# Kernel optimization log

Measured on AMD Instinct MI355X. Metric: run time of the kernel, lower is better.

## Reference

```python
import jax, jax.numpy as jnp
import numpy as np

B, D, K, S = 8192, 1024, 8192, 64  # batch, feature_dim, num_blocks, block_size
EPS = 1e-5


def layer_norm(x, g, b):
    mu = jnp.mean(x, axis=-1, keepdims=True)
    var = jnp.var(x, axis=-1, keepdims=True)
    return (x - mu) * jax.lax.rsqrt(var + EPS) * g + b


def setup_inputs() -> dict:
    key = jax.random.key(0)
    ks = jax.random.split(key, 12)
    s = 0.02
    return {
        "features": jax.random.normal(ks[0], (B, D), dtype=jnp.float32),
        "codebook": jax.random.normal(ks[1], (K, S), dtype=jnp.float32) * 0.1,
        # projection: Linear(D, 2S) -> ReLU -> LayerNorm(2S) -> Linear(2S, S)
        "proj_w1": jax.random.normal(ks[2], (D, 2 * S), dtype=jnp.float32) * s,
        "proj_b1": jnp.zeros((2 * S,), dtype=jnp.float32),
        "ln1_g": jnp.ones((2 * S,), dtype=jnp.float32),
        "ln1_b": jnp.zeros((2 * S,), dtype=jnp.float32),
        "proj_w2": jax.random.normal(ks[3], (2 * S, S), dtype=jnp.float32) * s,
        "proj_b2": jnp.zeros((S,), dtype=jnp.float32),
        # reconstruction: Linear(S, 2D) -> ReLU -> LayerNorm(2D) -> Linear(2D, D)
        "rec_w1": jax.random.normal(ks[4], (S, 2 * D), dtype=jnp.float32) * s,
        "rec_b1": jnp.zeros((2 * D,), dtype=jnp.float32),
        "ln2_g": jnp.ones((2 * D,), dtype=jnp.float32),
        "ln2_b": jnp.zeros((2 * D,), dtype=jnp.float32),
        "rec_w2": jax.random.normal(ks[5], (2 * D, D), dtype=jnp.float32) * s,
        "rec_b2": jnp.zeros((D,), dtype=jnp.float32),
    }


def reference(features, codebook, proj_w1, proj_b1, ln1_g, ln1_b, proj_w2, proj_b2,
              rec_w1, rec_b1, ln2_g, ln2_b, rec_w2, rec_b2):
    # --- encode ---
    h = jax.nn.relu(features @ proj_w1 + proj_b1)
    h = layer_norm(h, ln1_g, ln1_b)
    z = h @ proj_w2 + proj_b2  # [B, S] (dropout inactive in eval)
    # squared Euclidean distances; argmin identical to cdist(p=2) argmin
    d2 = (jnp.sum(z * z, axis=1, keepdims=True)
          - 2.0 * (z @ codebook.T)
          + jnp.sum(codebook * codebook, axis=1))  # [B, K]
    indices = jnp.argmin(d2, axis=1)  # [B]
    # usage scatter-add (buffer update in the torch module)
    block_usage = jnp.zeros((K,), dtype=jnp.float32).at[indices].add(1.0)
    # --- decode ---
    sel = codebook[indices]  # [B, S] embedding gather
    r = jax.nn.relu(sel @ rec_w1 + rec_b1)
    r = layer_norm(r, ln2_g, ln2_b)
    reconstructed = r @ rec_w2 + rec_b2  # [B, D]
    return reconstructed, indices, block_usage
```

## Files before the change

kernel.cpp:

```cpp
#include <hip/hip_runtime.h>
#include <hip/hip_bf16.h>
#include <stdint.h>

#define LN_EPS 1e-5f

typedef float f32x4 __attribute__((ext_vector_type(4)));
typedef short short8 __attribute__((ext_vector_type(8)));

__device__ __forceinline__ float bf2f(unsigned int u) {
  union { unsigned int i; float f; } x; x.i = u << 16; return x.f;
}
__device__ __forceinline__ unsigned short f2bf(float f) {
  unsigned int x = __float_as_uint(f);
  x += 0x7fffu + ((x >> 16) & 1u);
  return (unsigned short)(x >> 16);
}

__device__ __forceinline__ void gload16(const void* g, void* l) {
  __builtin_amdgcn_global_load_lds((const __attribute__((address_space(1))) unsigned int*)g,
                                   (__attribute__((address_space(3))) unsigned int*)l, 16, 0, 0);
}

__device__ __forceinline__ void stage_tile(const unsigned short* g, int ldg,
                                           unsigned short* lds, int wave, int lane) {
#pragma unroll
  for (int i = 0; i < 4; i++) {
    const int chunk = i * 4 + wave;
    const unsigned short* ga = g + (size_t)(chunk * 8 + (lane >> 3)) * ldg + (lane & 7) * 8;
    gload16(ga, lds + chunk * 512);
  }
}

__global__ __launch_bounds__(256) void k0_c2_zero(const float* __restrict__ CB,
                                                  float* __restrict__ C2,
                                                  float* __restrict__ usage) {
  const int g = blockIdx.x * 256 + threadIdx.x;
  const int code = g >> 4, l16 = g & 15;
  const float4 v = *(const float4*)&CB[(size_t)code * 64 + (l16 << 2)];
  float s = v.x * v.x + v.y * v.y + v.z * v.z + v.w * v.w;
#pragma unroll
  for (int m = 8; m >= 1; m >>= 1) s += __shfl_xor(s, m, 16);
  if (l16 == 0) C2[code] = s;
  if (g < 8192) usage[g] = 0.f;
}

__global__ __launch_bounds__(256) void k1_encode(const float* __restrict__ X,
                                                 const float* __restrict__ W1,
                                                 const float* __restrict__ B1,
                                                 const float* __restrict__ G1,
                                                 const float* __restrict__ Bn1,
                                                 const float* __restrict__ W2,
                                                 const float* __restrict__ B2,
                                                 float* __restrict__ Z) {
  __shared__ float At[64][20];
  __shared__ float Wc[64][128];
  __shared__ float Ht[128][20];
  const int t = threadIdx.x;
  const int row0 = blockIdx.x << 4;
  const int rg = t >> 6;
  const int r0 = rg << 2;
  const int cg = t & 63;
  const int c0 = cg << 1;
  const int lr = t >> 4, lkc = (t & 15) << 2;
  float acc[4][2] = {{0,0},{0,0},{0,0},{0,0}};

  for (int k0 = 0; k0 < 1024; k0 += 64) {
    __syncthreads();
    {
      const float4 av = *(const float4*)&X[(size_t)(row0 + lr) * 1024 + k0 + lkc];
      At[lkc + 0][lr] = av.x; At[lkc + 1][lr] = av.y;
      At[lkc + 2][lr] = av.z; At[lkc + 3][lr] = av.w;
    }
    {
      const float4* wsrc = (const float4*)&W1[(size_t)k0 * 128];
      float4* wdst = (float4*)&Wc[0][0];
#pragma unroll
      for (int i = 0; i < 8; i++) wdst[t + (i << 8)] = wsrc[t + (i << 8)];
    }
    __syncthreads();
#pragma unroll
    for (int kk = 0; kk < 64; kk++) {
      const float4 a = *(const float4*)&At[kk][r0];
      const float2 w = *(const float2*)&Wc[kk][c0];
      acc[0][0] = fmaf(a.x, w.x, acc[0][0]); acc[0][1] = fmaf(a.x, w.y, acc[0][1]);
      acc[1][0] = fmaf(a.y, w.x, acc[1][0]); acc[1][1] = fmaf(a.y, w.y, acc[1][1]);
      acc[2][0] = fmaf(a.z, w.x, acc[2][0]); acc[2][1] = fmaf(a.z, w.y, acc[2][1]);
      acc[3][0] = fmaf(a.w, w.x, acc[3][0]); acc[3][1] = fmaf(a.w, w.y, acc[3][1]);
    }
  }
  const float b1a = B1[c0], b1b = B1[c0 + 1];
  float h[4][2], s1[4], s2[4];
#pragma unroll
  for (int i = 0; i < 4; i++) {
    h[i][0] = fmaxf(acc[i][0] + b1a, 0.f);
    h[i][1] = fmaxf(acc[i][1] + b1b, 0.f);
    s1[i] = h[i][0] + h[i][1];
    s2[i] = h[i][0] * h[i][0] + h[i][1] * h[i][1];
  }
#pragma unroll
  for (int m = 32; m >= 1; m >>= 1) {
#pragma unroll
    for (int i = 0; i < 4; i++) { s1[i] += __shfl_xor(s1[i], m); s2[i] += __shfl_xor(s2[i], m); }
  }
  const float ga = G1[c0], gb = G1[c0 + 1], ba = Bn1[c0], bb = Bn1[c0 + 1];
#pragma unroll
  for (int i = 0; i < 4; i++) {
    const float mean = s1[i] * (1.f / 128.f);
    const float var  = s2[i] * (1.f / 128.f) - mean * mean;
    const float rs = rsqrtf(var + LN_EPS);
    Ht[c0 + 0][r0 + i] = (h[i][0] - mean) * rs * ga + ba;
    Ht[c0 + 1][r0 + i] = (h[i][1] - mean) * rs * gb + bb;
  }
  __syncthreads();
  float za[4] = {0, 0, 0, 0};
  for (int k = 0; k < 128; k++) {
    const float4 hv = *(const float4*)&Ht[k][r0];
    const float wv = W2[(k << 6) + cg];
    za[0] = fmaf(hv.x, wv, za[0]); za[1] = fmaf(hv.y, wv, za[1]);
    za[2] = fmaf(hv.z, wv, za[2]); za[3] = fmaf(hv.w, wv, za[3]);
  }
  const float b2v = B2[cg];
#pragma unroll
  for (int i = 0; i < 4; i++)
    Z[(size_t)(row0 + r0 + i) * 64 + cg] = za[i] + b2v;
}

__global__ __launch_bounds__(256) void k2_dist(const float* __restrict__ Z,
                                               const float* __restrict__ CB,
                                               const float* __restrict__ C2,
                                               float* __restrict__ Pval,
                                               int* __restrict__ Pidx) {
  __shared__ float Zt[64][36];
  __shared__ float Ct[2][64][132];
  const int t = threadIdx.x;
  const int lane = t & 63, wave = t >> 6;
  const int rowblk = blockIdx.x >> 1, half = blockIdx.x & 1;
  const int row0 = rowblk << 5;
  const int code0 = half << 12;
  const int rg = t >> 5;
  const int r0 = rg << 2;
  const int c0 = (lane & 31) << 2;

#pragma unroll
  for (int i = 0; i < 2; i++) {
    const int f = t + (i << 8);
    const int r = f >> 4, kc = (f & 15) << 2;
    const float4 v = *(const float4*)&Z[(size_t)(row0 + r) * 64 + kc];
    Zt[kc + 0][r] = v.x; Zt[kc + 1][r] = v.y;
    Zt[kc + 2][r] = v.z; Zt[kc + 3][r] = v.w;
  }

  const int wq = (wave << 4) + (lane >> 2);
  const int kb = (lane & 3) << 2;
  float4 st[8];
#define K2_PF(cr, r) \
  st[(cr) * 4 + (r)] = *(const float4*)&CB[(size_t)(code0 + chunk * 128 + (cr) * 64 + wq) * 64 + kb + 16 * (r)];
#define K2_WR(cr, r) { \
    const float4 v = st[(cr) * 4 + (r)]; \
    const int k2r = kb + 16 * (r); const int col = (cr) * 64 + wq; \
    Ct[buf][k2r + 0][col] = v.x; Ct[buf][k2r + 1][col] = v.y; \
    Ct[buf][k2r + 2][col] = v.z; Ct[buf][k2r + 3][col] = v.w; }

  {
    const int chunk = 0;
    K2_PF(0, 0) K2_PF(0, 1) K2_PF(0, 2) K2_PF(0, 3)
    K2_PF(1, 0) K2_PF(1, 1) K2_PF(1, 2) K2_PF(1, 3)
  }
  __syncthreads();

  float minv[4] = {3.4e38f, 3.4e38f, 3.4e38f, 3.4e38f};
  int   mini[4] = {0, 0, 0, 0};

  for (int c = 0; c < 32; c++) {
    const int buf = c & 1;
    K2_WR(0, 0) K2_WR(0, 1) K2_WR(0, 2) K2_WR(0, 3)
    K2_WR(1, 0) K2_WR(1, 1) K2_WR(1, 2) K2_WR(1, 3)
    __syncthreads();
    if (c + 1 < 32) {
      const int chunk = c + 1;
      K2_PF(0, 0) K2_PF(0, 1) K2_PF(0, 2) K2_PF(0, 3)
      K2_PF(1, 0) K2_PF(1, 1) K2_PF(1, 2) K2_PF(1, 3)
    }
    float acc[4][4];
#pragma unroll
    for (int i = 0; i < 4; i++)
#pragma unroll
      for (int j = 0; j < 4; j++) acc[i][j] = 0.f;
#pragma unroll 4
    for (int k = 0; k < 64; k++) {
      const float4 zv = *(const float4*)&Zt[k][r0];
      const float4 cv = *(const float4*)&Ct[buf][k][c0];
      acc[0][0] = fmaf(zv.x, cv.x, acc[0][0]); acc[0][1] = fmaf(zv.x, cv.y, acc[0][1]);
      acc[0][2] = fmaf(zv.x, cv.z, acc[0][2]); acc[0][3] = fmaf(zv.x, cv.w, acc[0][3]);
      acc[1][0] = fmaf(zv.y, cv.x, acc[1][0]); acc[1][1] = fmaf(zv.y, cv.y, acc[1][1]);
      acc[1][2] = fmaf(zv.y, cv.z, acc[1][2]); acc[1][3] = fmaf(zv.y, cv.w, acc[1][3]);
      acc[2][0] = fmaf(zv.z, cv.x, acc[2][0]); acc[2][1] = fmaf(zv.z, cv.y, acc[2][1]);
      acc[2][2] = fmaf(zv.z, cv.z, acc[2][2]); acc[2][3] = fmaf(zv.z, cv.w, acc[2][3]);
      acc[3][0] = fmaf(zv.w, cv.x, acc[3][0]); acc[3][1] = fmaf(zv.w, cv.y, acc[3][1]);
      acc[3][2] = fmaf(zv.w, cv.z, acc[3][2]); acc[3][3] = fmaf(zv.w, cv.w, acc[3][3]);
    }
    const int codeb = code0 + (c << 7) + c0;
    const float4 c2v = *(const float4*)&C2[codeb];
    const float c2a[4] = {c2v.x, c2v.y, c2v.z, c2v.w};
#pragma unroll
    for (int i = 0; i < 4; i++)
#pragma unroll
      for (int j = 0; j < 4; j++) {
        const float s = fmaf(-2.f, acc[i][j], c2a[j]);
        if (s < minv[i]) { minv[i] = s; mini[i] = codeb + j; }
      }
  }
#undef K2_PF
#undef K2_WR
#pragma unroll
  for (int m = 16; m >= 1; m >>= 1) {
#pragma unroll
    for (int i = 0; i < 4; i++) {
      const float ov = __shfl_xor(minv[i], m);
      const int   oi = __shfl_xor(mini[i], m);
      if (ov < minv[i] || (ov == minv[i] && oi < mini[i])) { minv[i] = ov; mini[i] = oi; }
    }
  }
  if ((lane & 31) == 0) {
#pragma unroll
    for (int i = 0; i < 4; i++) {
      const int r = row0 + r0 + i;
      Pval[r * 2 + half] = minv[i];
      Pidx[r * 2 + half] = mini[i];
    }
  }
}

__global__ __launch_bounds__(256) void k2_merge(const float* __restrict__ Pval,
                                                const int* __restrict__ Pidx,
                                                int* __restrict__ IDX,
                                                float* __restrict__ outIdx,
                                                float* __restrict__ usage) {
  const int r = blockIdx.x * 256 + threadIdx.x;
  const float v0 = Pval[r * 2], v1 = Pval[r * 2 + 1];
  const int i0 = Pidx[r * 2], i1 = Pidx[r * 2 + 1];
  const int best = (v1 < v0) ? i1 : i0;
  IDX[r] = best;
  outIdx[r] = (float)best;
  atomicAdd(&usage[best], 1.0f);
}

__global__ __launch_bounds__(256) void k_tcast(const float* __restrict__ src,
                                               unsigned short* __restrict__ dst,
                                               int R, int C) {
  __shared__ float T[32][33];
  const int tilesC = C >> 5;
  const int bx = blockIdx.x;
  const int tr = bx / tilesC, tc = bx - tr * tilesC;
  const int t = threadIdx.x;
  {
    const int r = t >> 3, c4 = (t & 7) << 2;
    const float4 v = *(const float4*)&src[(size_t)(tr * 32 + r) * C + tc * 32 + c4];
    T[r][c4] = v.x; T[r][c4 + 1] = v.y; T[r][c4 + 2] = v.z; T[r][c4 + 3] = v.w;
  }
  __syncthreads();
  const int c = t >> 3, r4 = (t & 7) << 2;
  ushort4 o;
  o.x = f2bf(T[r4 + 0][c]); o.y = f2bf(T[r4 + 1][c]);
  o.z = f2bf(T[r4 + 2][c]); o.w = f2bf(T[r4 + 3][c]);
  *(ushort4*)&dst[(size_t)(tc * 32 + c) * R + tr * 32 + r4] = o;
}

__global__ __launch_bounds__(256) void k3_gather(const float* __restrict__ CB,
                                                 const int* __restrict__ IDX,
                                                 unsigned short* __restrict__ SEL) {
  const int g = blockIdx.x * 256 + threadIdx.x;
  const int row = g >> 4, c4 = (g & 15) << 2;
  const int code = IDX[row];
  const float4 v = *(const float4*)&CB[(size_t)code * 64 + c4];
  ushort4 o;
  o.x = f2bf(v.x); o.y = f2bf(v.y); o.z = f2bf(v.z); o.w = f2bf(v.w);
  *(ushort4*)&SEL[(size_t)row * 64 + c4] = o;
}

__global__ __launch_bounds__(256) void k4_rec1(const unsigned short* __restrict__ A,
                                               const unsigned short* __restrict__ Bt,
                                               const float* __restrict__ bias,
                                               unsigned short* __restrict__ H) {
  __shared__ __align__(16) unsigned short As[128 * 64];
  __shared__ __align__(16) unsigned short Bs[128 * 64];
  const int t = threadIdx.x;
  const int wave = t >> 6, lane = t & 63;
  const int bx = blockIdx.x;
  const int tm = bx >> 4, tn = bx & 15;
  const int m0 = tm << 7, n0 = tn << 7;
  const int wm = wave >> 1, wn = wave & 1;
  const int ln15 = lane & 15, lk = (lane >> 4) << 3;
  stage_tile(A + (size_t)m0 * 64, 64, As, wave, lane);
  stage_tile(Bt + (size_t)n0 * 64, 64, Bs, wave, lane);
  asm volatile("s_waitcnt vmcnt(0)" ::: "memory");
  __syncthreads();
  f32x4 acc[4][4];
#pragma unroll
  for (int i = 0; i < 4; i++)
#pragma unroll
    for (int j = 0; j < 4; j++) acc[i][j] = (f32x4){0.f, 0.f, 0.f, 0.f};
#pragma unroll
  for (int ks = 0; ks < 2; ks++) {
    short8 a[4], b[4];
#pragma unroll
    for (int i = 0; i < 4; i++)
      a[i] = *(const short8*)&As[(wm * 64 + i * 16 + ln15) * 64 + ks * 32 + lk];
#pragma unroll
    for (int j = 0; j < 4; j++)
      b[j] = *(const short8*)&Bs[(wn * 64 + j * 16 + ln15) * 64 + ks * 32 + lk];
#pragma unroll
    for (int i = 0; i < 4; i++)
#pragma unroll
      for (int j = 0; j < 4; j++)
        acc[i][j] = __builtin_amdgcn_mfma_f32_16x16x32_bf16(a[i], b[j], acc[i][j], 0, 0, 0);
  }
  const int l4 = (lane >> 4) << 2;
#pragma unroll
  for (int j = 0; j < 4; j++) {
    const int col = n0 + wn * 64 + j * 16 + ln15;
    const float bv = bias[col];
#pragma unroll
    for (int i = 0; i < 4; i++) {
      const int row = m0 + wm * 64 + i * 16 + l4;
#pragma unroll
      for (int r = 0; r < 4; r++)
        H[(size_t)(row + r) * 2048 + col] = f2bf(fmaxf(acc[i][j][r] + bv, 0.f));
    }
  }
}

__global__ __launch_bounds__(256) void k5_ln(unsigned short* __restrict__ H,
                                             const float* __restrict__ G,
                                             const float* __restrict__ B) {
  const int row = blockIdx.x, t = threadIdx.x;
  unsigned short* p = H + (size_t)row * 2048 + t * 8;
  const uint4 raw = *(const uint4*)p;
  float v[8];
  v[0] = bf2f(raw.x & 0xffffu); v[1] = bf2f(raw.x >> 16);
  v[2] = bf2f(raw.y & 0xffffu); v[3] = bf2f(raw.y >> 16);
  v[4] = bf2f(raw.z & 0xffffu); v[5] = bf2f(raw.z >> 16);
  v[6] = bf2f(raw.w & 0xffffu); v[7] = bf2f(raw.w >> 16);
  float s1 = 0.f, s2 = 0.f;
#pragma unroll
  for (int i = 0; i < 8; i++) { s1 += v[i]; s2 = fmaf(v[i], v[i], s2); }
#pragma unroll
  for (int m = 32; m >= 1; m >>= 1) { s1 += __shfl_xor(s1, m); s2 += __shfl_xor(s2, m); }
  __shared__ float red[8];
  const int lane = t & 63, wv = t >> 6;
  if (lane == 0) { red[wv] = s1; red[4 + wv] = s2; }
  __syncthreads();
  s1 = red[0] + red[1] + red[2] + red[3];
  s2 = red[4] + red[5] + red[6] + red[7];
  const float mean = s1 * (1.f / 2048.f);
  const float var  = s2 * (1.f / 2048.f) - mean * mean;
  const float rs = rsqrtf(var + LN_EPS);
  const int c = t * 8;
  unsigned int w0, w1, w2, w3;
  {
    const float o0 = (v[0] - mean) * rs * G[c + 0] + B[c + 0];
    const float o1 = (v[1] - mean) * rs * G[c + 1] + B[c + 1];
    w0 = (unsigned int)f2bf(o0) | ((unsigned int)f2bf(o1) << 16);
  }
  {
    const float o0 = (v[2] - mean) * rs * G[c + 2] + B[c + 2];
    const float o1 = (v[3] - mean) * rs * G[c + 3] + B[c + 3];
    w1 = (unsigned int)f2bf(o0) | ((unsigned int)f2bf(o1) << 16);
  }
  {
    const float o0 = (v[4] - mean) * rs * G[c + 4] + B[c + 4];
    const float o1 = (v[5] - mean) * rs * G[c + 5] + B[c + 5];
    w2 = (unsigned int)f2bf(o0) | ((unsigned int)f2bf(o1) << 16);
  }
  {
    const float o0 = (v[6] - mean) * rs * G[c + 6] + B[c + 6];
    const float o1 = (v[7] - mean) * rs * G[c + 7] + B[c + 7];
    w3 = (unsigned int)f2bf(o0) | ((unsigned int)f2bf(o1) << 16);
  }
  uint4 outw; outw.x = w0; outw.y = w1; outw.z = w2; outw.w = w3;
  *(uint4*)p = outw;
}

__global__ __launch_bounds__(256) void k6_rec2(const unsigned short* __restrict__ A,
                                               const unsigned short* __restrict__ Bt,
                                               const float* __restrict__ bias,
                                               float* __restrict__ C) {
  __shared__ __align__(16) unsigned short As[128 * 64];
  __shared__ __align__(16) unsigned short Bs[128 * 64];
  const int t = threadIdx.x;
  const int wave = t >> 6, lane = t & 63;
  const int bx = blockIdx.x;
  const int tm = bx >> 3, tn = bx & 7;
  const int m0 = tm << 7, n0 = tn << 7;
  const int wm = wave >> 1, wn = wave & 1;
  const int ln15 = lane & 15, lk = (lane >> 4) << 3;
  f32x4 acc[4][4];
#pragma unroll
  for (int i = 0; i < 4; i++)
#pragma unroll
    for (int j = 0; j < 4; j++) acc[i][j] = (f32x4){0.f, 0.f, 0.f, 0.f};

  for (int k0 = 0; k0 < 2048; k0 += 64) {
    __syncthreads();
    stage_tile(A + (size_t)m0 * 2048 + k0, 2048, As, wave, lane);
    stage_tile(Bt + (size_t)n0 * 2048 + k0, 2048, Bs, wave, lane);
    asm volatile("s_waitcnt vmcnt(0)" ::: "memory");
    __syncthreads();
#pragma unroll
    for (int ks = 0; ks < 2; ks++) {
      short8 a[4], b[4];
#pragma unroll
      for (int i = 0; i < 4; i++)
        a[i] = *(const short8*)&As[(wm * 64 + i * 16 + ln15) * 64 + ks * 32 + lk];
#pragma unroll
      for (int j = 0; j < 4; j++)
        b[j] = *(const short8*)&Bs[(wn * 64 + j * 16 + ln15) * 64 + ks * 32 + lk];
#pragma unroll
      for (int i = 0; i < 4; i++)
#pragma unroll
        for (int j = 0; j < 4; j++)
          acc[i][j] = __builtin_amdgcn_mfma_f32_16x16x32_bf16(a[i], b[j], acc[i][j], 0, 0, 0);
    }
  }
  const int l4 = (lane >> 4) << 2;
#pragma unroll
  for (int j = 0; j < 4; j++) {
    const int col = n0 + wn * 64 + j * 16 + ln15;
    const float bv = bias[col];
#pragma unroll
    for (int i = 0; i < 4; i++) {
      const int row = m0 + wm * 64 + i * 16 + l4;
#pragma unroll
      for (int r = 0; r < 4; r++)
        C[(size_t)(row + r) * 1024 + col] = acc[i][j][r] + bv;
    }
  }
}

extern "C" void kernel_launch(void* const* d_in, const int* in_sizes, int n_in,
                              void* d_out, int out_size, void* d_ws, size_t ws_size,
                              hipStream_t stream) {
  (void)in_sizes; (void)n_in; (void)out_size; (void)ws_size;
  const float* features = (const float*)d_in[0];
  const float* codebook = (const float*)d_in[1];
  const float* proj_w1  = (const float*)d_in[2];
  const float* proj_b1  = (const float*)d_in[3];
  const float* ln1_g    = (const float*)d_in[4];
  const float* ln1_b    = (const float*)d_in[5];
  const float* proj_w2  = (const float*)d_in[6];
  const float* proj_b2  = (const float*)d_in[7];
  const float* rec_w1   = (const float*)d_in[8];
  const float* rec_b1   = (const float*)d_in[9];
  const float* ln2_g    = (const float*)d_in[10];
  const float* ln2_b    = (const float*)d_in[11];
  const float* rec_w2   = (const float*)d_in[12];
  const float* rec_b2   = (const float*)d_in[13];

  float* out_recon = (float*)d_out;
  float* out_idx   = out_recon + (size_t)8192 * 1024;
  float* out_usage = out_idx + 8192;

  char* ws = (char*)d_ws;
  float*          c2  = (float*)(ws);
  int*            idx = (int*)(ws + 32768);
  float*          z   = (float*)(ws + 65536);
  unsigned short* sel = (unsigned short*)(ws + 2162688);
  unsigned short* w1t = (unsigned short*)(ws + 3211264);
  unsigned short* w2t = (unsigned short*)(ws + 3473408);
  unsigned short* h1  = (unsigned short*)(ws + 7667712);
  float* pval = (float*)(ws + 2162688);
  int*   pidx = (int*)(ws + 2162688 + 65536);

  k0_c2_zero<<<512, 256, 0, stream>>>(codebook, c2, out_usage);
  k1_encode <<<512, 256, 0, stream>>>(features, proj_w1, proj_b1, ln1_g, ln1_b,
                                      proj_w2, proj_b2, z);
  k2_dist   <<<512, 256, 0, stream>>>(z, codebook, c2, pval, pidx);
  k2_merge  <<<32, 256, 0, stream>>>(pval, pidx, idx, out_idx, out_usage);
  k_tcast   <<<128, 256, 0, stream>>>(rec_w1, w1t, 64, 2048);
  k_tcast   <<<2048, 256, 0, stream>>>(rec_w2, w2t, 2048, 1024);
  k3_gather <<<512, 256, 0, stream>>>(codebook, idx, sel);
  k4_rec1   <<<1024, 256, 0, stream>>>(sel, w1t, rec_b1, h1);
  k5_ln     <<<8192, 256, 0, stream>>>(h1, ln2_g, ln2_b);
  k6_rec2   <<<512, 256, 0, stream>>>(h1, w2t, rec_b2, out_recon);
}
```

Before: 396.5 us.

## Split distance search into four code quarters and double-buffer rec2 GEMM tiles

The distance kernel now splits the codebook into four quarters per row block instead of two, which doubles the grid to 1024 blocks. Its LDS tile becomes single-buffered with an extra barrier, cutting shared memory per block so more blocks can be resident. The merge kernel reduces four partial minima using vector loads. The rec2 MFMA GEMM gains double-buffered LDS staging so the next K tile loads while the current one computes, at the cost of twice the LDS footprint.

```diff
diff --git a/kernel.cpp b/kernel.cpp
--- a/kernel.cpp
+++ b/kernel.cpp
@@ -130,15 +130,14 @@
                                                const float* __restrict__ C2,
                                                float* __restrict__ Pval,
                                                int* __restrict__ Pidx) {
-  __shared__ float Zt[64][36];
-  __shared__ float Ct[2][64][132];
+  __shared__ float Zt[64][34];
+  __shared__ float Ct[64][130];
   const int t = threadIdx.x;
   const int lane = t & 63, wave = t >> 6;
-  const int rowblk = blockIdx.x >> 1, half = blockIdx.x & 1;
+  const int rowblk = blockIdx.x >> 2, quarter = blockIdx.x & 3;
   const int row0 = rowblk << 5;
-  const int code0 = half << 12;
-  const int rg = t >> 5;
-  const int r0 = rg << 2;
+  const int code0 = quarter << 11;
+  const int r0 = (t >> 5) << 2;
   const int c0 = (lane & 31) << 2;
 
 #pragma unroll
@@ -158,8 +157,8 @@
 #define K2_WR(cr, r) { \
     const float4 v = st[(cr) * 4 + (r)]; \
     const int k2r = kb + 16 * (r); const int col = (cr) * 64 + wq; \
-    Ct[buf][k2r + 0][col] = v.x; Ct[buf][k2r + 1][col] = v.y; \
-    Ct[buf][k2r + 2][col] = v.z; Ct[buf][k2r + 3][col] = v.w; }
+    Ct[k2r + 0][col] = v.x; Ct[k2r + 1][col] = v.y; \
+    Ct[k2r + 2][col] = v.z; Ct[k2r + 3][col] = v.w; }
 
   {
     const int chunk = 0;
@@ -171,12 +170,11 @@
   float minv[4] = {3.4e38f, 3.4e38f, 3.4e38f, 3.4e38f};
   int   mini[4] = {0, 0, 0, 0};
 
-  for (int c = 0; c < 32; c++) {
-    const int buf = c & 1;
+  for (int c = 0; c < 16; c++) {
     K2_WR(0, 0) K2_WR(0, 1) K2_WR(0, 2) K2_WR(0, 3)
     K2_WR(1, 0) K2_WR(1, 1) K2_WR(1, 2) K2_WR(1, 3)
     __syncthreads();
-    if (c + 1 < 32) {
+    if (c + 1 < 16) {
       const int chunk = c + 1;
       K2_PF(0, 0) K2_PF(0, 1) K2_PF(0, 2) K2_PF(0, 3)
       K2_PF(1, 0) K2_PF(1, 1) K2_PF(1, 2) K2_PF(1, 3)
@@ -189,7 +187,7 @@
 #pragma unroll 4
     for (int k = 0; k < 64; k++) {
       const float4 zv = *(const float4*)&Zt[k][r0];
-      const float4 cv = *(const float4*)&Ct[buf][k][c0];
+      const float4 cv = *(const float4*)&Ct[k][c0];
       acc[0][0] = fmaf(zv.x, cv.x, acc[0][0]); acc[0][1] = fmaf(zv.x, cv.y, acc[0][1]);
       acc[0][2] = fmaf(zv.x, cv.z, acc[0][2]); acc[0][3] = fmaf(zv.x, cv.w, acc[0][3]);
       acc[1][0] = fmaf(zv.y, cv.x, acc[1][0]); acc[1][1] = fmaf(zv.y, cv.y, acc[1][1]);
@@ -209,6 +207,7 @@
         const float s = fmaf(-2.f, acc[i][j], c2a[j]);
         if (s < minv[i]) { minv[i] = s; mini[i] = codeb + j; }
       }
+    __syncthreads();
   }
 #undef K2_PF
 #undef K2_WR
@@ -225,8 +224,8 @@
 #pragma unroll
     for (int i = 0; i < 4; i++) {
       const int r = row0 + r0 + i;
-      Pval[r * 2 + half] = minv[i];
-      Pidx[r * 2 + half] = mini[i];
+      Pval[r * 4 + quarter] = minv[i];
+      Pidx[r * 4 + quarter] = mini[i];
     }
   }
 }
@@ -237,12 +236,15 @@
                                                 float* __restrict__ outIdx,
                                                 float* __restrict__ usage) {
   const int r = blockIdx.x * 256 + threadIdx.x;
-  const float v0 = Pval[r * 2], v1 = Pval[r * 2 + 1];
-  const int i0 = Pidx[r * 2], i1 = Pidx[r * 2 + 1];
-  const int best = (v1 < v0) ? i1 : i0;
-  IDX[r] = best;
-  outIdx[r] = (float)best;
-  atomicAdd(&usage[best], 1.0f);
+  const float4 v = *(const float4*)&Pval[r * 4];
+  const int4   i = *(const int4*)&Pidx[r * 4];
+  float bv = v.x; int bi = i.x;
+  if (v.y < bv) { bv = v.y; bi = i.y; }
+  if (v.z < bv) { bv = v.z; bi = i.z; }
+  if (v.w < bv) { bv = v.w; bi = i.w; }
+  IDX[r] = bi;
+  outIdx[r] = (float)bi;
+  atomicAdd(&usage[bi], 1.0f);
 }
 
 __global__ __launch_bounds__(256) void k_tcast(const float* __restrict__ src,
@@ -385,8 +387,8 @@
                                                const unsigned short* __restrict__ Bt,
                                                const float* __restrict__ bias,
                                                float* __restrict__ C) {
-  __shared__ __align__(16) unsigned short As[128 * 64];
-  __shared__ __align__(16) unsigned short Bs[128 * 64];
+  __shared__ __align__(16) unsigned short As[2][128 * 64];
+  __shared__ __align__(16) unsigned short Bs[2][128 * 64];
   const int t = threadIdx.x;
   const int wave = t >> 6, lane = t & 63;
   const int bx = blockIdx.x;
@@ -400,27 +402,36 @@
 #pragma unroll
     for (int j = 0; j < 4; j++) acc[i][j] = (f32x4){0.f, 0.f, 0.f, 0.f};
 
-  for (int k0 = 0; k0 < 2048; k0 += 64) {
-    __syncthreads();
-    stage_tile(A + (size_t)m0 * 2048 + k0, 2048, As, wave, lane);
-    stage_tile(Bt + (size_t)n0 * 2048 + k0, 2048, Bs, wave, lane);
+  stage_tile(A + (size_t)m0 * 2048, 2048, As[0], wave, lane);
+  stage_tile(Bt + (size_t)n0 * 2048, 2048, Bs[0], wave, lane);
+  asm volatile("s_waitcnt vmcnt(0)" ::: "memory");
+  __syncthreads();
+
+  int cur = 0;
+  for (int kt = 0; kt < 32; kt++) {
+    if (kt + 1 < 32) {
+      const int k0 = (kt + 1) << 6;
+      stage_tile(A + (size_t)m0 * 2048 + k0, 2048, As[cur ^ 1], wave, lane);
+      stage_tile(Bt + (size_t)n0 * 2048 + k0, 2048, Bs[cur ^ 1], wave, lane);
+    }
+#pragma unroll
+    for (int ks = 0; ks < 2; ks++) {
+      short8 a[4], b[4];
+#pragma unroll
+      for (int i = 0; i < 4; i++)
+        a[i] = *(const short8*)&As[cur][(wm * 64 + i * 16 + ln15) * 64 + ks * 32 + lk];
+#pragma unroll
+      for (int j = 0; j < 4; j++)
+        b[j] = *(const short8*)&Bs[cur][(wn * 64 + j * 16 + ln15) * 64 + ks * 32 + lk];
+#pragma unroll
+      for (int i = 0; i < 4; i++)
+#pragma unroll
+        for (int j = 0; j < 4; j++)
+          acc[i][j] = __builtin_amdgcn_mfma_f32_16x16x32_bf16(a[i], b[j], acc[i][j], 0, 0, 0);
+    }
     asm volatile("s_waitcnt vmcnt(0)" ::: "memory");
     __syncthreads();
-#pragma unroll
-    for (int ks = 0; ks < 2; ks++) {
-      short8 a[4], b[4];
-#pragma unroll
-      for (int i = 0; i < 4; i++)
-        a[i] = *(const short8*)&As[(wm * 64 + i * 16 + ln15) * 64 + ks * 32 + lk];
-#pragma unroll
-      for (int j = 0; j < 4; j++)
-        b[j] = *(const short8*)&Bs[(wn * 64 + j * 16 + ln15) * 64 + ks * 32 + lk];
-#pragma unroll
-      for (int i = 0; i < 4; i++)
-#pragma unroll
-        for (int j = 0; j < 4; j++)
-          acc[i][j] = __builtin_amdgcn_mfma_f32_16x16x32_bf16(a[i], b[j], acc[i][j], 0, 0, 0);
-    }
+    cur ^= 1;
   }
   const int l4 = (lane >> 4) << 2;
 #pragma unroll
@@ -469,12 +480,12 @@
   unsigned short* w2t = (unsigned short*)(ws + 3473408);
   unsigned short* h1  = (unsigned short*)(ws + 7667712);
   float* pval = (float*)(ws + 2162688);
-  int*   pidx = (int*)(ws + 2162688 + 65536);
+  int*   pidx = (int*)(ws + 2162688 + 131072);
 
   k0_c2_zero<<<512, 256, 0, stream>>>(codebook, c2, out_usage);
   k1_encode <<<512, 256, 0, stream>>>(features, proj_w1, proj_b1, ln1_g, ln1_b,
                                       proj_w2, proj_b2, z);
-  k2_dist   <<<512, 256, 0, stream>>>(z, codebook, c2, pval, pidx);
+  k2_dist   <<<1024, 256, 0, stream>>>(z, codebook, c2, pval, pidx);
   k2_merge  <<<32, 256, 0, stream>>>(pval, pidx, idx, out_idx, out_usage);
   k_tcast   <<<128, 256, 0, stream>>>(rec_w1, w1t, 64, 2048);
   k_tcast   <<<2048, 256, 0, stream>>>(rec_w2, w2t, 2048, 1024);
```

Measured after the change: 427.5 us. +7.8%, slower.
